# Kernel optimization log

Hardware: AMD Instinct MI355X
Metric: run time of the kernel (lower is better)

The kernel has to match this reference:

```python
import jax, jax.numpy as jnp
import numpy as np

T = 8388608          # sequence length (inputs reshaped to (1, T, 1) in original)
HALF_WIDTH = 0.5     # Phi hard-codes tf.constant([[1/2.0]]) regardless of width arg


def phi(v):
    # Phi(v) = v - 0.5 if v > 0.5 ; v + 0.5 if v < -0.5 ; 0 otherwise
    return jnp.where(v > HALF_WIDTH, v - HALF_WIDTH,
                     jnp.where(v < -HALF_WIDTH, v + HALF_WIDTH, jnp.zeros_like(v)))


def setup_inputs() -> dict:
    key = jax.random.key(0)
    k1, k2 = jax.random.split(key)
    x = jax.random.normal(k1, (1, T), dtype=jnp.float32)
    # learned kernel, shape (1,1), non_neg constraint -> positive init
    weight = jax.random.uniform(k2, (1, 1), dtype=jnp.float32, minval=0.5, maxval=1.5)
    state0 = jnp.zeros((1, 1), dtype=jnp.float32)
    return {"x": x, "weight": weight, "state0": state0}


def reference(x, weight, state0):
    # scale inputs by scalar kernel, flatten to the time axis: (T,)
    xs = (x * weight[0, 0]).reshape(-1)

    def step(s, xt):
        o = phi(xt - s) + s   # hysteresis update: output is also the new state
        return o, o

    s_last, outs = jax.lax.scan(step, state0[0, 0], xs)
    outputs = outs.reshape(1, T, 1)          # matches tf.keras.backend.rnn outputs_
    final_state = s_last.reshape(1, 1)       # matches states_x[-1]
    return outputs, final_state
```

## Files before the change

kernel.cpp:

```cpp
#include <hip/hip_runtime.h>
#include <math.h>


#define T_ELEMS 8388608
#define BLOCK   256
#define EPT     4
#define EPB     (BLOCK * EPT)
#define NBLK    (T_ELEMS / EPB)
#define P2T     256
#define P2PER   (NBLK / P2T)

#define NEG_INF (-__builtin_inff())
#define POS_INF (__builtin_inff())

struct Op { float lo, hi; };

__device__ __forceinline__ Op combine(Op a, Op b) {
    Op r;
    r.lo = fmaxf(b.lo, fminf(b.hi, a.lo));
    r.hi = fminf(b.hi, a.hi);
    return r;
}

__device__ __forceinline__ float apply_op(Op o, float s) {
    return fmaxf(o.lo, fminf(o.hi, s));
}

__device__ __forceinline__ void fold_elem(Op& t, float e) {
    float elo = e - 0.5f, ehi = e + 0.5f;
    t.lo = fmaxf(elo, fminf(ehi, t.lo));
    t.hi = fminf(ehi, t.hi);
}

__device__ __forceinline__ Op thread_op(float4 v) {
    Op t = { v.x - 0.5f, v.x + 0.5f };
    fold_elem(t, v.y);
    fold_elem(t, v.z);
    fold_elem(t, v.w);
    return t;
}

__device__ __forceinline__ Op wave_incl_scan(Op t, int lane) {
#pragma unroll
    for (int off = 1; off < 64; off <<= 1) {
        float nlo = __shfl_up(t.lo, off);
        float nhi = __shfl_up(t.hi, off);
        if (lane >= off) {
            Op prev = { nlo, nhi };
            t = combine(prev, t);
        }
    }
    return t;
}

__device__ __forceinline__ Op block_excl_from_incl(Op incl, int lane, int wid, Op* lds_wt) {
    if (lane == 63) lds_wt[wid] = incl;
    __syncthreads();
    Op wpre = { NEG_INF, POS_INF };
    for (int k = 0; k < wid; ++k) wpre = combine(wpre, lds_wt[k]);
    float elo = __shfl_up(incl.lo, 1);
    float ehi = __shfl_up(incl.hi, 1);
    Op excl;
    if (lane == 0) { excl.lo = NEG_INF; excl.hi = POS_INF; }
    else           { excl.lo = elo;     excl.hi = ehi;     }
    return combine(wpre, excl);
}

__global__ __launch_bounds__(BLOCK) void phase1(const float* __restrict__ x,
                                                const float* __restrict__ w,
                                                float2* __restrict__ blkTot) {
    __shared__ Op wt[BLOCK / 64];
    const float wv = w[0];
    const int tid = threadIdx.x;
    const size_t base = (size_t)blockIdx.x * EPB + (size_t)tid * EPT;
    float4 v = *reinterpret_cast<const float4*>(x + base);
    v.x *= wv; v.y *= wv; v.z *= wv; v.w *= wv;
    Op t = thread_op(v);

#pragma unroll
    for (int off = 1; off < 64; off <<= 1) {
        float nlo = __shfl_down(t.lo, off);
        float nhi = __shfl_down(t.hi, off);
        Op nb = { nlo, nhi };
        t = combine(t, nb);
    }
    if ((tid & 63) == 0) wt[tid >> 6] = t;
    __syncthreads();
    if (tid == 0) {
        Op b = wt[0];
#pragma unroll
        for (int k = 1; k < BLOCK / 64; ++k) b = combine(b, wt[k]);
        blkTot[blockIdx.x] = make_float2(b.lo, b.hi);
    }
}

__global__ __launch_bounds__(P2T) void phase2(const float2* __restrict__ blkTot,
                                              const float* __restrict__ state0,
                                              float* __restrict__ blkStart,
                                              float* __restrict__ finalOut) {
    __shared__ Op wt[P2T / 64];
    const int tid = threadIdx.x;
    const int lane = tid & 63, wid = tid >> 6;

    Op t = { NEG_INF, POS_INF };
#pragma unroll 4
    for (int j = 0; j < P2PER; ++j) {
        float2 b = blkTot[tid * P2PER + j];
        Op o = { b.x, b.y };
        t = combine(t, o);
    }

    Op incl = wave_incl_scan(t, lane);
    Op myex = block_excl_from_incl(incl, lane, wid, wt);

    float s = apply_op(myex, state0[0]);
#pragma unroll 4
    for (int j = 0; j < P2PER; ++j) {
        blkStart[tid * P2PER + j] = s;
        float2 b = blkTot[tid * P2PER + j];
        Op o = { b.x, b.y };
        s = apply_op(o, s);
    }
    if (tid == P2T - 1) finalOut[0] = s;
}

__global__ __launch_bounds__(BLOCK) void phase3(const float* __restrict__ x,
                                                const float* __restrict__ w,
                                                const float* __restrict__ blkStart,
                                                float* __restrict__ out) {
    __shared__ Op wt[BLOCK / 64];
    const float wv = w[0];
    const int tid = threadIdx.x;
    const int lane = tid & 63, wid = tid >> 6;
    const size_t base = (size_t)blockIdx.x * EPB + (size_t)tid * EPT;
    float4 v = *reinterpret_cast<const float4*>(x + base);
    v.x *= wv; v.y *= wv; v.z *= wv; v.w *= wv;

    Op t = thread_op(v);
    Op incl = wave_incl_scan(t, lane);
    Op myex = block_excl_from_incl(incl, lane, wid, wt);

    float s = apply_op(myex, blkStart[blockIdx.x]);

    float4 o;
    s = fmaxf(v.x - 0.5f, fminf(v.x + 0.5f, s)); o.x = s;
    s = fmaxf(v.y - 0.5f, fminf(v.y + 0.5f, s)); o.y = s;
    s = fmaxf(v.z - 0.5f, fminf(v.z + 0.5f, s)); o.z = s;
    s = fmaxf(v.w - 0.5f, fminf(v.w + 0.5f, s)); o.w = s;
    *reinterpret_cast<float4*>(out + base) = o;
}

extern "C" void kernel_launch(void* const* d_in, const int* in_sizes, int n_in,
                              void* d_out, int out_size, void* d_ws, size_t ws_size,
                              hipStream_t stream) {
    const float* x  = (const float*)d_in[0];
    const float* w  = (const float*)d_in[1];
    const float* s0 = (const float*)d_in[2];
    float* out = (float*)d_out;

    float2* blkTot   = (float2*)d_ws;
    float*  blkStart = (float*)((char*)d_ws + NBLK * sizeof(float2));

    phase1<<<NBLK, BLOCK, 0, stream>>>(x, w, blkTot);
    phase2<<<1, P2T, 0, stream>>>(blkTot, s0, blkStart, out + T_ELEMS);
    phase3<<<NBLK, BLOCK, 0, stream>>>(x, w, blkStart, out);
}
```

Baseline: 102.6 us.

## Merge scan phases into two kernels with larger per-thread tiles and LDS transpose

Drops the single-block middle scan kernel. Each apply block now reduces all preceding block aggregates itself, so only two launches remain. Per-thread work rises to 32 elements, loaded coalesced and transposed through swizzled LDS, which cuts the block count to 1024 and the number of aggregates. The cost is redundant prefix work in every block (up to 4 aggregates per thread) and extra LDS traffic.

```diff
diff --git a/kernel.cpp b/kernel.cpp
--- a/kernel.cpp
+++ b/kernel.cpp
@@ -3,15 +3,17 @@
 
 
 #define T_ELEMS 8388608
-#define BLOCK   256
-#define EPT     4
-#define EPB     (BLOCK * EPT)
-#define NBLK    (T_ELEMS / EPB)
-#define P2T     256
-#define P2PER   (NBLK / P2T)
-
 #define NEG_INF (-__builtin_inff())
 #define POS_INF (__builtin_inff())
+
+#define BLOCK   256
+#define WAVES   4
+#define F4T     8
+#define F4W     (64 * F4T)
+#define F4B     (BLOCK * F4T)
+#define EPB     (F4B * 4)
+#define NBLK    (T_ELEMS / EPB)
+#define APT     (NBLK / BLOCK)
 
 struct Op { float lo, hi; };
 
@@ -21,24 +23,18 @@
     r.hi = fminf(b.hi, a.hi);
     return r;
 }
-
 __device__ __forceinline__ float apply_op(Op o, float s) {
     return fmaxf(o.lo, fminf(o.hi, s));
 }
-
 __device__ __forceinline__ void fold_elem(Op& t, float e) {
     float elo = e - 0.5f, ehi = e + 0.5f;
     t.lo = fmaxf(elo, fminf(ehi, t.lo));
     t.hi = fminf(ehi, t.hi);
 }
-
-__device__ __forceinline__ Op thread_op(float4 v) {
-    Op t = { v.x - 0.5f, v.x + 0.5f };
-    fold_elem(t, v.y);
-    fold_elem(t, v.z);
-    fold_elem(t, v.w);
-    return t;
+__device__ __forceinline__ void fold4(Op& t, float4 v) {
+    fold_elem(t, v.x); fold_elem(t, v.y); fold_elem(t, v.z); fold_elem(t, v.w);
 }
+__device__ __forceinline__ int swz(int idx) { return idx ^ ((idx >> 3) & 7); }
 
 __device__ __forceinline__ Op wave_incl_scan(Op t, int lane) {
 #pragma unroll
@@ -52,102 +48,135 @@
     }
     return t;
 }
+__device__ __forceinline__ Op wave_reduce(Op t) {
+#pragma unroll
+    for (int off = 1; off < 64; off <<= 1) {
+        Op nb;
+        nb.lo = __shfl_down(t.lo, off);
+        nb.hi = __shfl_down(t.hi, off);
+        t = combine(t, nb);
+    }
+    return t;
+}
 
-__device__ __forceinline__ Op block_excl_from_incl(Op incl, int lane, int wid, Op* lds_wt) {
-    if (lane == 63) lds_wt[wid] = incl;
+__device__ __forceinline__ void load_tile(const float4* __restrict__ xg,
+                                          size_t wbase, int lane, float wv,
+                                          float4* wbuf, float4 v[F4T]) {
+#pragma unroll
+    for (int j = 0; j < F4T; ++j) {
+        float4 t = xg[wbase + j * 64 + lane];
+        t.x *= wv; t.y *= wv; t.z *= wv; t.w *= wv;
+        wbuf[swz(j * 64 + lane)] = t;
+    }
+#pragma unroll
+    for (int k = 0; k < F4T; ++k)
+        v[k] = wbuf[swz(lane * F4T + k)];
+}
+
+__global__ __launch_bounds__(BLOCK) void k1_agg(const float* __restrict__ x,
+                                                const float* __restrict__ w,
+                                                float2* __restrict__ agg) {
+    __shared__ float4 xbuf[WAVES * F4W];
+    __shared__ Op wt[WAVES];
+    const int tid = threadIdx.x, lane = tid & 63, wid = tid >> 6;
+    const int b = blockIdx.x;
+    const float wv = w[0];
+
+    float4* wbuf = xbuf + wid * F4W;
+    const size_t wbase = (size_t)b * F4B + (size_t)wid * F4W;
+    const float4* xg = reinterpret_cast<const float4*>(x);
+
+    float4 v[F4T];
+    load_tile(xg, wbase, lane, wv, wbuf, v);
+
+    Op t = { v[0].x - 0.5f, v[0].x + 0.5f };
+    fold_elem(t, v[0].y); fold_elem(t, v[0].z); fold_elem(t, v[0].w);
+#pragma unroll
+    for (int k = 1; k < F4T; ++k) fold4(t, v[k]);
+
+    t = wave_reduce(t);
+    if (lane == 0) wt[wid] = t;
     __syncthreads();
+    if (tid == 0) {
+        Op bt = wt[0];
+#pragma unroll
+        for (int k = 1; k < WAVES; ++k) bt = combine(bt, wt[k]);
+        agg[b] = make_float2(bt.lo, bt.hi);
+    }
+}
+
+__global__ __launch_bounds__(BLOCK) void k2_apply(const float* __restrict__ x,
+                                                  const float* __restrict__ w,
+                                                  const float* __restrict__ s0,
+                                                  const float2* __restrict__ agg,
+                                                  float* __restrict__ out) {
+    __shared__ float4 xbuf[WAVES * F4W];
+    __shared__ Op wtA[WAVES];
+    __shared__ Op wtP[WAVES];
+    const int tid = threadIdx.x, lane = tid & 63, wid = tid >> 6;
+    const int b = blockIdx.x;
+    const float wv = w[0];
+
+    Op seg = { NEG_INF, POS_INF };
+#pragma unroll
+    for (int j = 0; j < APT; ++j) {
+        int i = tid * APT + j;
+        if (i < b) {
+            float2 f = agg[i];
+            Op o = { f.x, f.y };
+            seg = combine(seg, o);
+        }
+    }
+    seg = wave_reduce(seg);
+    if (lane == 0) wtP[wid] = seg;
+
+    float4* wbuf = xbuf + wid * F4W;
+    const size_t wbase = (size_t)b * F4B + (size_t)wid * F4W;
+    const float4* xg = reinterpret_cast<const float4*>(x);
+
+    float4 v[F4T];
+    load_tile(xg, wbase, lane, wv, wbuf, v);
+
+    Op t = { v[0].x - 0.5f, v[0].x + 0.5f };
+    fold_elem(t, v[0].y); fold_elem(t, v[0].z); fold_elem(t, v[0].w);
+#pragma unroll
+    for (int k = 1; k < F4T; ++k) fold4(t, v[k]);
+
+    Op incl = wave_incl_scan(t, lane);
+    if (lane == 63) wtA[wid] = incl;
+    __syncthreads();
+
+    Op Eb = wtP[0];
+#pragma unroll
+    for (int k = 1; k < WAVES; ++k) Eb = combine(Eb, wtP[k]);
+
     Op wpre = { NEG_INF, POS_INF };
-    for (int k = 0; k < wid; ++k) wpre = combine(wpre, lds_wt[k]);
+    for (int k = 0; k < wid; ++k) wpre = combine(wpre, wtA[k]);
     float elo = __shfl_up(incl.lo, 1);
     float ehi = __shfl_up(incl.hi, 1);
     Op excl;
     if (lane == 0) { excl.lo = NEG_INF; excl.hi = POS_INF; }
     else           { excl.lo = elo;     excl.hi = ehi;     }
-    return combine(wpre, excl);
-}
 
-__global__ __launch_bounds__(BLOCK) void phase1(const float* __restrict__ x,
-                                                const float* __restrict__ w,
-                                                float2* __restrict__ blkTot) {
-    __shared__ Op wt[BLOCK / 64];
-    const float wv = w[0];
-    const int tid = threadIdx.x;
-    const size_t base = (size_t)blockIdx.x * EPB + (size_t)tid * EPT;
-    float4 v = *reinterpret_cast<const float4*>(x + base);
-    v.x *= wv; v.y *= wv; v.z *= wv; v.w *= wv;
-    Op t = thread_op(v);
+    float s = apply_op(Eb, s0[0]);
+    s = apply_op(combine(wpre, excl), s);
 
+    float4* og = reinterpret_cast<float4*>(out);
 #pragma unroll
-    for (int off = 1; off < 64; off <<= 1) {
-        float nlo = __shfl_down(t.lo, off);
-        float nhi = __shfl_down(t.hi, off);
-        Op nb = { nlo, nhi };
-        t = combine(t, nb);
+    for (int k = 0; k < F4T; ++k) {
+        float4 e = v[k], o4;
+        s = fmaxf(e.x - 0.5f, fminf(e.x + 0.5f, s)); o4.x = s;
+        s = fmaxf(e.y - 0.5f, fminf(e.y + 0.5f, s)); o4.y = s;
+        s = fmaxf(e.z - 0.5f, fminf(e.z + 0.5f, s)); o4.z = s;
+        s = fmaxf(e.w - 0.5f, fminf(e.w + 0.5f, s)); o4.w = s;
+        wbuf[swz(lane * F4T + k)] = o4;
     }
-    if ((tid & 63) == 0) wt[tid >> 6] = t;
-    __syncthreads();
-    if (tid == 0) {
-        Op b = wt[0];
 #pragma unroll
-        for (int k = 1; k < BLOCK / 64; ++k) b = combine(b, wt[k]);
-        blkTot[blockIdx.x] = make_float2(b.lo, b.hi);
-    }
-}
+    for (int j = 0; j < F4T; ++j)
+        og[wbase + j * 64 + lane] = wbuf[swz(j * 64 + lane)];
 
-__global__ __launch_bounds__(P2T) void phase2(const float2* __restrict__ blkTot,
-                                              const float* __restrict__ state0,
-                                              float* __restrict__ blkStart,
-                                              float* __restrict__ finalOut) {
-    __shared__ Op wt[P2T / 64];
-    const int tid = threadIdx.x;
-    const int lane = tid & 63, wid = tid >> 6;
-
-    Op t = { NEG_INF, POS_INF };
-#pragma unroll 4
-    for (int j = 0; j < P2PER; ++j) {
-        float2 b = blkTot[tid * P2PER + j];
-        Op o = { b.x, b.y };
-        t = combine(t, o);
-    }
-
-    Op incl = wave_incl_scan(t, lane);
-    Op myex = block_excl_from_incl(incl, lane, wid, wt);
-
-    float s = apply_op(myex, state0[0]);
-#pragma unroll 4
-    for (int j = 0; j < P2PER; ++j) {
-        blkStart[tid * P2PER + j] = s;
-        float2 b = blkTot[tid * P2PER + j];
-        Op o = { b.x, b.y };
-        s = apply_op(o, s);
-    }
-    if (tid == P2T - 1) finalOut[0] = s;
-}
-
-__global__ __launch_bounds__(BLOCK) void phase3(const float* __restrict__ x,
-                                                const float* __restrict__ w,
-                                                const float* __restrict__ blkStart,
-                                                float* __restrict__ out) {
-    __shared__ Op wt[BLOCK / 64];
-    const float wv = w[0];
-    const int tid = threadIdx.x;
-    const int lane = tid & 63, wid = tid >> 6;
-    const size_t base = (size_t)blockIdx.x * EPB + (size_t)tid * EPT;
-    float4 v = *reinterpret_cast<const float4*>(x + base);
-    v.x *= wv; v.y *= wv; v.z *= wv; v.w *= wv;
-
-    Op t = thread_op(v);
-    Op incl = wave_incl_scan(t, lane);
-    Op myex = block_excl_from_incl(incl, lane, wid, wt);
-
-    float s = apply_op(myex, blkStart[blockIdx.x]);
-
-    float4 o;
-    s = fmaxf(v.x - 0.5f, fminf(v.x + 0.5f, s)); o.x = s;
-    s = fmaxf(v.y - 0.5f, fminf(v.y + 0.5f, s)); o.y = s;
-    s = fmaxf(v.z - 0.5f, fminf(v.z + 0.5f, s)); o.z = s;
-    s = fmaxf(v.w - 0.5f, fminf(v.w + 0.5f, s)); o.w = s;
-    *reinterpret_cast<float4*>(out + base) = o;
+    if (b == NBLK - 1 && tid == BLOCK - 1)
+        out[T_ELEMS] = s;
 }
 
 extern "C" void kernel_launch(void* const* d_in, const int* in_sizes, int n_in,
@@ -158,10 +187,8 @@
     const float* s0 = (const float*)d_in[2];
     float* out = (float*)d_out;
 
-    float2* blkTot   = (float2*)d_ws;
-    float*  blkStart = (float*)((char*)d_ws + NBLK * sizeof(float2));
+    float2* agg = (float2*)d_ws;
 
-    phase1<<<NBLK, BLOCK, 0, stream>>>(x, w, blkTot);
-    phase2<<<1, P2T, 0, stream>>>(blkTot, s0, blkStart, out + T_ELEMS);
-    phase3<<<NBLK, BLOCK, 0, stream>>>(x, w, blkStart, out);
+    k1_agg<<<NBLK, BLOCK, 0, stream>>>(x, w, agg);
+    k2_apply<<<NBLK, BLOCK, 0, stream>>>(x, w, s0, agg, out);
 }
```

New measurement: 92.34 us. -10.0%, faster.
